# Kernel tuning notes

Measured on AMD Instinct MI355X. Metric: run time of the kernel, lower is better.

The kernel has to match this reference:

```python
import jax, jax.numpy as jnp
import numpy as np

B, S, D, H, N = 8, 1024, 1024, 16, 16  # batch, seq, hidden, heads, num_ns_tokens
HD = D // H


def setup_inputs() -> dict:
    key = jax.random.key(0)
    ks = jax.random.split(key, 8)
    s = 0.02
    return {
        "x": jax.random.normal(ks[0], (B, S, D), jnp.float32),
        "Wq_shared": jax.random.normal(ks[1], (D, D), jnp.float32) * s,
        "Wk_shared": jax.random.normal(ks[2], (D, D), jnp.float32) * s,
        "Wv_shared": jax.random.normal(ks[3], (D, D), jnp.float32) * s,
        "Wq_ded": jax.random.normal(ks[4], (N, D, D), jnp.float32) * s,
        "Wk_ded": jax.random.normal(ks[5], (N, D, D), jnp.float32) * s,
        "Wv_ded": jax.random.normal(ks[6], (N, D, D), jnp.float32) * s,
        "Wo": jax.random.normal(ks[7], (D, D), jnp.float32) * s,
    }


def reference(x, Wq_shared, Wk_shared, Wv_shared, Wq_ded, Wk_ded, Wv_ded, Wo):
    b, s, d = x.shape
    n = Wq_ded.shape[0]

    def proj(Ws, Wd):
        shared = x @ Ws                                   # [b,s,d]
        ded = jnp.einsum('bnd,ndo->bno', x[:, :n], Wd)    # first n tokens use dedicated weights
        return jnp.concatenate([ded, shared[:, n:]], axis=1)

    q = proj(Wq_shared, Wq_ded).reshape(b, s, H, HD)
    k = proj(Wk_shared, Wk_ded).reshape(b, s, H, HD)
    v = proj(Wv_shared, Wv_ded).reshape(b, s, H, HD)

    scores = jnp.einsum('bqhd,bkhd->bhqk', q, k) / jnp.sqrt(jnp.float32(HD))
    causal = jnp.tril(jnp.ones((s, s), dtype=bool))
    scores = jnp.where(causal, scores, jnp.float32(-1e9))
    attn = jax.nn.softmax(scores, axis=-1)
    out = jnp.einsum('bhqk,bkhd->bqhd', attn, v).reshape(b, s, d)
    output = out @ Wo
    return (output, k, v)
```

## Files before the change

kernel.cpp:

```cpp
#include <hip/hip_runtime.h>
#include <cstdint>


typedef unsigned short u16;
typedef __attribute__((ext_vector_type(8)))  __bf16 bf16x8;
typedef __attribute__((ext_vector_type(8)))  u16    u16x8;
typedef __attribute__((ext_vector_type(4)))  float  f32x4;

#define BSD   (8u * 1024u * 1024u)
#define QSCALE 0.18033688011112042f

__device__ __forceinline__ u16 f2bf(float f) {
    unsigned u = __builtin_bit_cast(unsigned, f);
    u += 0x7fffu + ((u >> 16) & 1u);
    return (u16)(u >> 16);
}

__device__ __forceinline__ unsigned pack_bf2(float p0, float p1) {
    return __builtin_amdgcn_perm(__builtin_bit_cast(unsigned, p1),
                                 __builtin_bit_cast(unsigned, p0), 0x07060302u);
}

__device__ __forceinline__ void gl_lds16(const void* g, void* l) {
    __builtin_amdgcn_global_load_lds(
        (const __attribute__((address_space(1))) unsigned*)g,
        (__attribute__((address_space(3))) unsigned*)l, 16, 0, 0);
}

__global__ __launch_bounds__(256) void cvt_fused(
        const float* __restrict__ Wq, const float* __restrict__ Wk,
        const float* __restrict__ Wv, const float* __restrict__ Wo,
        u16* __restrict__ WTcat, u16* __restrict__ WoT,
        const float4* __restrict__ x, u16* __restrict__ xb) {
    __shared__ float t[32][33];
    int z = blockIdx.z;
    if (z < 4) {
        const float* src = (z == 0) ? Wq : (z == 1) ? Wk : (z == 2) ? Wv : Wo;
        u16* dst = (z < 3) ? (WTcat + (size_t)z * 1024 * 1024) : WoT;
        int k0 = blockIdx.x * 32, n0 = blockIdx.y * 32;
        int xx = threadIdx.x & 31, yy = threadIdx.x >> 5;
#pragma unroll
        for (int i = 0; i < 4; ++i)
            t[yy + 8 * i][xx] = src[(size_t)(k0 + yy + 8 * i) * 1024 + n0 + xx];
        __syncthreads();
#pragma unroll
        for (int i = 0; i < 4; ++i)
            dst[(size_t)(n0 + yy + 8 * i) * 1024 + k0 + xx] = f2bf(t[xx][yy + 8 * i]);
    } else {
        int lb = (z - 4) * 1024 + blockIdx.y * 32 + blockIdx.x;
        int i = lb * 256 + threadIdx.x;
        float4 v = x[i];
        ushort4 o;
        o.x = f2bf(v.x); o.y = f2bf(v.y); o.z = f2bf(v.z); o.w = f2bf(v.w);
        ((ushort4*)xb)[i] = o;
    }
}

template <int MODE>
__global__ __launch_bounds__(256) void gemm128(
        const u16* __restrict__ A, const u16* __restrict__ Bt,
        float* __restrict__ fout, u16* __restrict__ q_attn,
        u16* __restrict__ k_attn) {
    const int K = 1024;
    __shared__ u16 As[128 * 64];
    __shared__ u16 Bs[128 * 64];
    int tid = threadIdx.x;
    int wave = tid >> 6, lane = tid & 63;
    int m0 = blockIdx.y * 128, n0 = blockIdx.x * 128;
    int wm = wave & 1, wn = wave >> 1;
    int lr = lane & 15, kg = lane >> 4;

    f32x4 acc[4][4] = {};

    for (int k0 = 0; k0 < K; k0 += 64) {
        __syncthreads();
#pragma unroll
        for (int j = 0; j < 4; ++j) {
            int ci = j * 256 + tid;
            int row = ci >> 3, cg = (ci & 7) ^ (row & 7);
            gl_lds16(A  + (size_t)(m0 + row) * K + k0 + cg * 8, As + ci * 8);
            gl_lds16(Bt + (size_t)(n0 + row) * K + k0 + cg * 8, Bs + ci * 8);
        }
        __syncthreads();
#pragma unroll
        for (int ks = 0; ks < 2; ++ks) {
            bf16x8 af[4], bf[4];
#pragma unroll
            for (int i = 0; i < 4; ++i) {
                int row = wm * 64 + i * 16 + lr;
                af[i] = __builtin_bit_cast(bf16x8,
                    *(const u16x8*)&As[row * 64 + (((ks * 4 + kg) ^ (row & 7)) * 8)]);
            }
#pragma unroll
            for (int j = 0; j < 4; ++j) {
                int row = wn * 64 + j * 16 + lr;
                bf[j] = __builtin_bit_cast(bf16x8,
                    *(const u16x8*)&Bs[row * 64 + (((ks * 4 + kg) ^ (row & 7)) * 8)]);
            }
#pragma unroll
            for (int i = 0; i < 4; ++i)
#pragma unroll
                for (int j = 0; j < 4; ++j)
                    acc[i][j] = __builtin_amdgcn_mfma_f32_16x16x32_bf16(
                        af[i], bf[j], acc[i][j], 0, 0, 0);
        }
    }

    if (MODE == 1) {
#pragma unroll
        for (int i = 0; i < 4; ++i) {
            int mbase = m0 + wm * 64 + i * 16 + kg * 4;
#pragma unroll
            for (int j = 0; j < 4; ++j) {
                int col = n0 + wn * 64 + j * 16 + lr;
#pragma unroll
                for (int r = 0; r < 4; ++r)
                    fout[(size_t)(mbase + r) * 1024 + col] = acc[i][j][r];
            }
        }
    } else {
        int matId = n0 >> 10;
        int ncol0 = (n0 & 1023) + wn * 64;
#pragma unroll
        for (int i = 0; i < 4; ++i) {
            int mbase = m0 + wm * 64 + i * 16 + kg * 4;
#pragma unroll
            for (int j = 0; j < 4; ++j) {
                int col = ncol0 + j * 16 + lr;
#pragma unroll
                for (int r = 0; r < 4; ++r) {
                    int mm = mbase + r;
                    float v = acc[i][j][r];
                    size_t idx = (size_t)mm * 1024 + col;
                    if (matId == 0) {
                        q_attn[idx] = f2bf(v * QSCALE);
                    } else if (matId == 1) {
                        fout[(size_t)BSD + idx] = v;
                        k_attn[idx] = f2bf(v);
                    } else {
                        fout[(size_t)2 * BSD + idx] = v;
                    }
                }
            }
        }
    }
}

__global__ __launch_bounds__(256) void ded_partial(
        const float* __restrict__ x, const float* __restrict__ Wq,
        const float* __restrict__ Wk, const float* __restrict__ Wv,
        float* __restrict__ part) {
    int dc = blockIdx.x, n = blockIdx.y, mat = blockIdx.z;
    const float* W = ((mat == 0) ? Wq : (mat == 1) ? Wk : Wv) +
                     (size_t)n * 1024 * 1024;
    __shared__ float xs[8 * 128];
    int t = threadIdx.x;
    for (int i = t; i < 1024; i += 256) {
        int b = i >> 7, d = i & 127;
        xs[i] = x[((size_t)b * 1024 + n) * 1024 + dc * 128 + d];
    }
    __syncthreads();
    int o0 = t * 4;
    float4 acc[8];
#pragma unroll
    for (int b = 0; b < 8; ++b) acc[b] = make_float4(0.f, 0.f, 0.f, 0.f);
    for (int d = 0; d < 128; d += 4) {
        float4 w0 = *(const float4*)&W[(size_t)(dc * 128 + d + 0) * 1024 + o0];
        float4 w1 = *(const float4*)&W[(size_t)(dc * 128 + d + 1) * 1024 + o0];
        float4 w2 = *(const float4*)&W[(size_t)(dc * 128 + d + 2) * 1024 + o0];
        float4 w3 = *(const float4*)&W[(size_t)(dc * 128 + d + 3) * 1024 + o0];
#pragma unroll
        for (int b = 0; b < 8; ++b) {
            float x0 = xs[b * 128 + d], x1 = xs[b * 128 + d + 1];
            float x2 = xs[b * 128 + d + 2], x3 = xs[b * 128 + d + 3];
            acc[b].x += x0 * w0.x + x1 * w1.x + x2 * w2.x + x3 * w3.x;
            acc[b].y += x0 * w0.y + x1 * w1.y + x2 * w2.y + x3 * w3.y;
            acc[b].z += x0 * w0.z + x1 * w1.z + x2 * w2.z + x3 * w3.z;
            acc[b].w += x0 * w0.w + x1 * w1.w + x2 * w2.w + x3 * w3.w;
        }
    }
#pragma unroll
    for (int b = 0; b < 8; ++b)
        *(float4*)&part[(size_t)(((mat * 8 + dc) * 8 + b) * 16 + n) * 1024 + o0] = acc[b];
}

__global__ __launch_bounds__(256) void fix_vt(
        const float* __restrict__ part, float* __restrict__ d_out,
        u16* __restrict__ q_attn, u16* __restrict__ k_attn,
        const float* __restrict__ vf, u16* __restrict__ vT) {
    __shared__ float t[64][65];
    int bid = blockIdx.x;
    int tid = threadIdx.x;

    if (bid < 384) {
        int mat = bid >> 7, b = (bid >> 4) & 7, n = bid & 15;
        int o0 = tid * 4;
        float v[4] = {0.f, 0.f, 0.f, 0.f};
        for (int dc = 0; dc < 8; ++dc) {
            float4 p = *(const float4*)&part[(size_t)(((mat * 8 + dc) * 8 + b) * 16 + n) * 1024 + o0];
            v[0] += p.x; v[1] += p.y; v[2] += p.z; v[3] += p.w;
        }
#pragma unroll
        for (int j = 0; j < 4; ++j) {
            int col = o0 + j;
            size_t idx = ((size_t)b * 1024 + n) * 1024 + col;
            if (mat == 0) {
                q_attn[idx] = f2bf(v[j] * QSCALE);
            } else if (mat == 1) {
                d_out[(size_t)BSD + idx] = v[j];
                k_attn[idx] = f2bf(v[j]);
            } else {
                d_out[(size_t)2 * BSD + idx] = v[j];
                int h = col >> 6, hd = col & 63;
                vT[((size_t)((b * 16 + h) * 64 + hd)) * 1024 + n] = f2bf(v[j]);
            }
        }
        return;
    }

    int id = bid - 384;
    int st = id & 15, h = (id >> 4) & 15, b = id >> 8;
    int cg = tid & 15, sl = tid >> 4;
#pragma unroll
    for (int p = 0; p < 4; ++p) {
        int s = p * 16 + sl;
        float4 v = *(const float4*)&vf[
            ((size_t)(b * 1024 + st * 64 + s)) * 1024 + h * 64 + cg * 4];
        t[cg * 4 + 0][s] = v.x;
        t[cg * 4 + 1][s] = v.y;
        t[cg * 4 + 2][s] = v.z;
        t[cg * 4 + 3][s] = v.w;
    }
    __syncthreads();
    int hd = tid >> 2, sc = (tid & 3) * 16;
    if (st == 0 && sc == 0) return;
    u16* dst = vT + ((size_t)((b * 16 + h) * 64 + hd)) * 1024 + st * 64 + sc;
#pragma unroll
    for (int c = 0; c < 4; ++c) {
        ushort4 o;
        o.x = f2bf(t[hd][sc + c * 4 + 0]);
        o.y = f2bf(t[hd][sc + c * 4 + 1]);
        o.z = f2bf(t[hd][sc + c * 4 + 2]);
        o.w = f2bf(t[hd][sc + c * 4 + 3]);
        *(ushort4*)(dst + c * 4) = o;
    }
}

__global__ __launch_bounds__(256) void attn(
        const u16* __restrict__ q_attn, const u16* __restrict__ k_attn,
        const u16* __restrict__ vT, u16* __restrict__ O) {
    int qt = 7 - blockIdx.x;
    int h = blockIdx.y, b = blockIdx.z;
    const u16* Qg = q_attn + ((size_t)(b * 1024) + qt * 128) * 1024 + h * 64;
    const u16* Kg = k_attn + ((size_t)(b * 1024)) * 1024 + h * 64;
    const u16* Vg = vT + (size_t)((b * 16 + h) * 64) * 1024;

    __shared__ u16 Qs[128 * 64];
    __shared__ u16 Ks[64 * 64];
    __shared__ u16 Vs[64 * 64];
    __shared__ u16 Ps[128 * 64];
    __shared__ float red[4 * 32];

    int tid = threadIdx.x, wave = tid >> 6, lane = tid & 63;
    int lr = lane & 15, kg = lane >> 4;

#pragma unroll
    for (int j = 0; j < 4; ++j) {
        int ci = j * 256 + tid;
        int row = ci >> 3, cg = (ci & 7) ^ (row & 7);
        gl_lds16(Qg + (size_t)row * 1024 + cg * 8, Qs + ci * 8);
    }

    float l_acc[2] = {0.f, 0.f};
    f32x4 oacc[2][4] = {};

    int nkt = 2 * qt + 2;
    for (int kt = 0; kt < nkt; ++kt) {
        __syncthreads();
#pragma unroll
        for (int j = 0; j < 2; ++j) {
            int ci = j * 256 + tid;
            int row = ci >> 3, cg = (ci & 7) ^ (row & 7);
            gl_lds16(Kg + (size_t)(kt * 64 + row) * 1024 + cg * 8, Ks + ci * 8);
            gl_lds16(Vg + (size_t)row * 1024 + kt * 64 + cg * 8, Vs + ci * 8);
        }
        __syncthreads();

        bool wactive = (qt * 128 + wave * 32 + 31) >= kt * 64;
        if (wactive) {
            f32x4 sacc[4][2] = {};
#pragma unroll
            for (int ks = 0; ks < 2; ++ks) {
                bf16x8 af[4], bq[2];
#pragma unroll
                for (int mi = 0; mi < 4; ++mi) {
                    int row = mi * 16 + lr;
                    af[mi] = __builtin_bit_cast(bf16x8,
                        *(const u16x8*)&Ks[row * 64 + (((ks * 4 + kg) ^ (row & 7)) * 8)]);
                }
#pragma unroll
                for (int nj = 0; nj < 2; ++nj) {
                    int qr = wave * 32 + nj * 16 + lr;
                    bq[nj] = __builtin_bit_cast(bf16x8,
                        *(const u16x8*)&Qs[qr * 64 + (((ks * 4 + kg) ^ (qr & 7)) * 8)]);
                }
#pragma unroll
                for (int mi = 0; mi < 4; ++mi)
#pragma unroll
                    for (int nj = 0; nj < 2; ++nj)
                        sacc[mi][nj] = __builtin_amdgcn_mfma_f32_16x16x32_bf16(
                            af[mi], bq[nj], sacc[mi][nj], 0, 0, 0);
            }

            if (kt >= 2 * qt) {
#pragma unroll
                for (int mi = 0; mi < 4; ++mi)
#pragma unroll
                    for (int nj = 0; nj < 2; ++nj)
#pragma unroll
                        for (int r = 0; r < 4; ++r) {
                            int kk_g = kt * 64 + mi * 16 + kg * 4 + r;
                            int q_g  = qt * 128 + wave * 32 + nj * 16 + lr;
                            if (kk_g > q_g) sacc[mi][nj][r] = -1e30f;
                        }
            }

#pragma unroll
            for (int nj = 0; nj < 2; ++nj) {
                int q = wave * 32 + nj * 16 + lr;
                float lsum = 0.f;
#pragma unroll
                for (int mi = 0; mi < 4; ++mi) {
                    float p0 = __builtin_amdgcn_exp2f(sacc[mi][nj][0]);
                    float p1 = __builtin_amdgcn_exp2f(sacc[mi][nj][1]);
                    float p2 = __builtin_amdgcn_exp2f(sacc[mi][nj][2]);
                    float p3 = __builtin_amdgcn_exp2f(sacc[mi][nj][3]);
                    lsum += (p0 + p1) + (p2 + p3);
                    int kkc = mi * 2 + (kg >> 1);
                    int off = q * 64 + ((kkc ^ (q & 7)) * 8) + (kg & 1) * 4;
                    uint2 w2;
                    w2.x = pack_bf2(p0, p1);
                    w2.y = pack_bf2(p2, p3);
                    *(uint2*)&Ps[off] = w2;
                }
                l_acc[nj] += lsum;
            }

#pragma unroll
            for (int ks = 0; ks < 2; ++ks) {
                bf16x8 ap[2], bv[4];
#pragma unroll
                for (int mi = 0; mi < 2; ++mi) {
                    int q = wave * 32 + mi * 16 + lr;
                    ap[mi] = __builtin_bit_cast(bf16x8,
                        *(const u16x8*)&Ps[q * 64 + (((ks * 4 + kg) ^ (q & 7)) * 8)]);
                }
#pragma unroll
                for (int nj = 0; nj < 4; ++nj) {
                    int hd = nj * 16 + lr;
                    bv[nj] = __builtin_bit_cast(bf16x8,
                        *(const u16x8*)&Vs[hd * 64 + (((ks * 4 + kg) ^ (hd & 7)) * 8)]);
                }
#pragma unroll
                for (int mi = 0; mi < 2; ++mi)
#pragma unroll
                    for (int nj = 0; nj < 4; ++nj)
                        oacc[mi][nj] = __builtin_amdgcn_mfma_f32_16x16x32_bf16(
                            ap[mi], bv[nj], oacc[mi][nj], 0, 0, 0);
            }
        }
    }

#pragma unroll
    for (int nj = 0; nj < 2; ++nj) {
        float l = l_acc[nj];
        l += __shfl_xor(l, 16);
        l += __shfl_xor(l, 32);
        if (kg == 0) red[wave * 32 + nj * 16 + lr] = l;
    }
#pragma unroll
    for (int mi = 0; mi < 2; ++mi) {
        f32x4 lv = *(f32x4*)&red[wave * 32 + mi * 16 + kg * 4];
        f32x4 rv;
#pragma unroll
        for (int r = 0; r < 4; ++r) rv[r] = __builtin_amdgcn_rcpf(lv[r]);
#pragma unroll
        for (int nj = 0; nj < 4; ++nj)
#pragma unroll
            for (int r = 0; r < 4; ++r) {
                int q_local = wave * 32 + mi * 16 + kg * 4 + r;
                size_t row = (size_t)b * 1024 + qt * 128 + q_local;
                O[row * 1024 + h * 64 + nj * 16 + lr] =
                    f2bf(oacc[mi][nj][r] * rv[r]);
            }
    }
}

extern "C" void kernel_launch(void* const* d_in, const int* in_sizes, int n_in,
                              void* d_out, int out_size, void* d_ws, size_t ws_size,
                              hipStream_t stream) {
    const float* x   = (const float*)d_in[0];
    const float* Wq  = (const float*)d_in[1];
    const float* Wk  = (const float*)d_in[2];
    const float* Wv  = (const float*)d_in[3];
    const float* Wqd = (const float*)d_in[4];
    const float* Wkd = (const float*)d_in[5];
    const float* Wvd = (const float*)d_in[6];
    const float* Wo  = (const float*)d_in[7];
    float* out = (float*)d_out;

    char* ws = (char*)d_ws;
    u16*   WTcat  = (u16*)(ws);
    u16*   WoT    = (u16*)(ws + 6291456);
    u16*   xb     = (u16*)(ws + 8388608);
    u16*   q_attn = (u16*)(ws + 25165824);
    u16*   k_attn = (u16*)(ws + 41943040);
    u16*   vT     = (u16*)(ws + 58720256);
    u16*   Ow     = (u16*)(ws + 75497472);
    float* part   = (float*)(ws + 92274688);

    cvt_fused<<<dim3(32, 32, 12), 256, 0, stream>>>(
        Wq, Wk, Wv, Wo, WTcat, WoT, (const float4*)x, xb);
    gemm128<0><<<dim3(24, 64), 256, 0, stream>>>(xb, WTcat, out, q_attn, k_attn);
    ded_partial<<<dim3(8, 16, 3), 256, 0, stream>>>(x, Wqd, Wkd, Wvd, part);
    fix_vt<<<dim3(2432), 256, 0, stream>>>(
        part, out, q_attn, k_attn, out + (size_t)2 * BSD, vT);
    attn<<<dim3(8, 16, 8), 256, 0, stream>>>(q_attn, k_attn, vT, Ow);
    gemm128<1><<<dim3(8, 64), 256, 0, stream>>>(Ow, WoT, out, nullptr, nullptr);
}
```

Before: 462.7 us.

## Replace GEMM with 8-wave double-buffered 128x256 tile ping-pong pipeline

Replaces the 4-wave 128x128 single-buffered GEMM with an 8-wave 128x256 tile kernel that double-buffers LDS. Global-to-LDS loads for the next K-step are split into four phases and interleaved with MFMA quarters, gated by explicit vmcnt waits, barriers and setprio. The aim is to hide global load latency behind compute and raise reuse per tile. In exchange it uses more LDS (96KB per block, which limits occupancy) and more barriers per K-step, and the hand-tuned waitcnt schedule is fragile.

Measured after the change: 474.3 us. 2.5% more time.

```diff
diff --git a/kernel.cpp b/kernel.cpp
--- a/kernel.cpp
+++ b/kernel.cpp
@@ -26,6 +26,9 @@
         (const __attribute__((address_space(1))) unsigned*)g,
         (__attribute__((address_space(3))) unsigned*)l, 16, 0, 0);
 }
+
+#define FENCE asm volatile("" ::: "memory")
+#define WAITV(n) asm volatile("s_waitcnt vmcnt(" #n ")" ::: "memory")
 
 __global__ __launch_bounds__(256) void cvt_fused(
         const float* __restrict__ Wq, const float* __restrict__ Wk,
@@ -56,81 +59,113 @@
     }
 }
 
+#define LDfrag(BUF, bufi, row, ks)                                            \
+    __builtin_bit_cast(bf16x8, *(const u16x8*)&BUF[bufi]                      \
+        [(row) * 64 + ((((ks) * 4 + kg) ^ ((row) & 7)) * 8)])
+
+#define PH(bufi, mh, nh, STAGE_STMT, GATE_STMT) do {                          \
+    bf16x8 af_[2][2], bq_[2][2];                                              \
+    _Pragma("unroll") for (int mi = 0; mi < 2; ++mi) {                        \
+        int arow = wm * 64 + (mh) * 32 + mi * 16 + lr;                        \
+        _Pragma("unroll") for (int ks = 0; ks < 2; ++ks)                      \
+            af_[mi][ks] = LDfrag(As, bufi, arow, ks);                         \
+    }                                                                         \
+    _Pragma("unroll") for (int ni = 0; ni < 2; ++ni) {                        \
+        int brow = wn * 64 + (nh) * 32 + ni * 16 + lr;                        \
+        _Pragma("unroll") for (int ks = 0; ks < 2; ++ks)                      \
+            bq_[ni][ks] = LDfrag(Bs, bufi, brow, ks);                         \
+    }                                                                         \
+    STAGE_STMT;                                                               \
+    GATE_STMT;                                                                \
+    FENCE; __builtin_amdgcn_s_barrier(); FENCE;                               \
+    asm volatile("s_waitcnt lgkmcnt(0)" ::: "memory");                        \
+    __builtin_amdgcn_s_setprio(1);                                            \
+    _Pragma("unroll") for (int ks = 0; ks < 2; ++ks)                          \
+    _Pragma("unroll") for (int mi = 0; mi < 2; ++mi)                          \
+    _Pragma("unroll") for (int ni = 0; ni < 2; ++ni)                          \
+        acc[(mh) * 2 + mi][(nh) * 2 + ni] =                                   \
+            __builtin_amdgcn_mfma_f32_16x16x32_bf16(                          \
+                af_[mi][ks], bq_[ni][ks],                                     \
+                acc[(mh) * 2 + mi][(nh) * 2 + ni], 0, 0, 0);                  \
+    __builtin_amdgcn_s_setprio(0);                                            \
+    FENCE; __builtin_amdgcn_s_barrier(); FENCE;                               \
+} while (0)
+
 template <int MODE>
-__global__ __launch_bounds__(256) void gemm128(
+__global__ __launch_bounds__(512, 2) void gemm8p(
         const u16* __restrict__ A, const u16* __restrict__ Bt,
         float* __restrict__ fout, u16* __restrict__ q_attn,
         u16* __restrict__ k_attn) {
-    const int K = 1024;
-    __shared__ u16 As[128 * 64];
-    __shared__ u16 Bs[128 * 64];
+    const int K = 1024, nt = 16;
+    __shared__ u16 As[2][128 * 64];
+    __shared__ u16 Bs[2][256 * 64];
     int tid = threadIdx.x;
-    int wave = tid >> 6, lane = tid & 63;
-    int m0 = blockIdx.y * 128, n0 = blockIdx.x * 128;
-    int wm = wave & 1, wn = wave >> 1;
+    int w = tid >> 6, lane = tid & 63;
+    int m0 = blockIdx.y * 128, n0 = blockIdx.x * 256;
+    int wm = w & 1, wn = w >> 1;
     int lr = lane & 15, kg = lane >> 4;
 
     f32x4 acc[4][4] = {};
 
-    for (int k0 = 0; k0 < K; k0 += 64) {
-        __syncthreads();
-#pragma unroll
-        for (int j = 0; j < 4; ++j) {
-            int ci = j * 256 + tid;
+    auto stageA = [&](int buf, int half, int t) {
+        int ci = ((w & 3) << 6) + lane + ((w >> 2) << 9) + (half << 8);
+        int row = ci >> 3, cg = (ci & 7) ^ (row & 7);
+        gl_lds16(A + (size_t)(m0 + row) * K + t * 64 + cg * 8, &As[buf][ci * 8]);
+    };
+    auto stageB = [&](int buf, int half, int t) {
+#pragma unroll
+        for (int j = 0; j < 2; ++j) {
+            int u = w + 8 * j;
+            int ci = ((u >> 2) << 9) + ((u & 3) << 6) + lane + (half << 8);
             int row = ci >> 3, cg = (ci & 7) ^ (row & 7);
-            gl_lds16(A  + (size_t)(m0 + row) * K + k0 + cg * 8, As + ci * 8);
-            gl_lds16(Bt + (size_t)(n0 + row) * K + k0 + cg * 8, Bs + ci * 8);
-        }
-        __syncthreads();
-#pragma unroll
-        for (int ks = 0; ks < 2; ++ks) {
-            bf16x8 af[4], bf[4];
-#pragma unroll
-            for (int i = 0; i < 4; ++i) {
-                int row = wm * 64 + i * 16 + lr;
-                af[i] = __builtin_bit_cast(bf16x8,
-                    *(const u16x8*)&As[row * 64 + (((ks * 4 + kg) ^ (row & 7)) * 8)]);
-            }
-#pragma unroll
-            for (int j = 0; j < 4; ++j) {
-                int row = wn * 64 + j * 16 + lr;
-                bf[j] = __builtin_bit_cast(bf16x8,
-                    *(const u16x8*)&Bs[row * 64 + (((ks * 4 + kg) ^ (row & 7)) * 8)]);
-            }
-#pragma unroll
-            for (int i = 0; i < 4; ++i)
-#pragma unroll
-                for (int j = 0; j < 4; ++j)
-                    acc[i][j] = __builtin_amdgcn_mfma_f32_16x16x32_bf16(
-                        af[i], bf[j], acc[i][j], 0, 0, 0);
-        }
-    }
+            gl_lds16(Bt + (size_t)(n0 + row) * K + t * 64 + cg * 8, &Bs[buf][ci * 8]);
+        }
+    };
+
+    stageA(0, 0, 0);
+    stageB(0, 0, 0);
+    stageA(0, 1, 0);
+    stageB(0, 1, 0);
+    WAITV(3);
+    FENCE; __builtin_amdgcn_s_barrier(); FENCE;
+
+    for (int t = 0; t < nt - 1; ++t) {
+        int cur = t & 1, nxt = cur ^ 1;
+        PH(cur, 0, 0, stageA(nxt, 0, t + 1), WAITV(3));
+        PH(cur, 1, 0, stageB(nxt, 0, t + 1), WAITV(3));
+        PH(cur, 1, 1, stageA(nxt, 1, t + 1), ((void)0));
+        PH(cur, 0, 1, stageB(nxt, 1, t + 1), WAITV(3));
+    }
+    PH(1, 0, 0, ((void)0), WAITV(2));
+    PH(1, 1, 0, ((void)0), WAITV(0));
+    PH(1, 1, 1, ((void)0), ((void)0));
+    PH(1, 0, 1, ((void)0), ((void)0));
 
     if (MODE == 1) {
 #pragma unroll
-        for (int i = 0; i < 4; ++i) {
-            int mbase = m0 + wm * 64 + i * 16 + kg * 4;
-#pragma unroll
-            for (int j = 0; j < 4; ++j) {
-                int col = n0 + wn * 64 + j * 16 + lr;
+        for (int am = 0; am < 4; ++am) {
+            int mbase = m0 + wm * 64 + am * 16 + kg * 4;
+#pragma unroll
+            for (int bn = 0; bn < 4; ++bn) {
+                int col = n0 + wn * 64 + bn * 16 + lr;
 #pragma unroll
                 for (int r = 0; r < 4; ++r)
-                    fout[(size_t)(mbase + r) * 1024 + col] = acc[i][j][r];
+                    fout[(size_t)(mbase + r) * 1024 + col] = acc[am][bn][r];
             }
         }
     } else {
         int matId = n0 >> 10;
         int ncol0 = (n0 & 1023) + wn * 64;
 #pragma unroll
-        for (int i = 0; i < 4; ++i) {
-            int mbase = m0 + wm * 64 + i * 16 + kg * 4;
-#pragma unroll
-            for (int j = 0; j < 4; ++j) {
-                int col = ncol0 + j * 16 + lr;
+        for (int am = 0; am < 4; ++am) {
+            int mbase = m0 + wm * 64 + am * 16 + kg * 4;
+#pragma unroll
+            for (int bn = 0; bn < 4; ++bn) {
+                int col = ncol0 + bn * 16 + lr;
 #pragma unroll
                 for (int r = 0; r < 4; ++r) {
                     int mm = mbase + r;
-                    float v = acc[i][j][r];
+                    float v = acc[am][bn][r];
                     size_t idx = (size_t)mm * 1024 + col;
                     if (matId == 0) {
                         q_attn[idx] = f2bf(v * QSCALE);
@@ -421,10 +456,10 @@
 
     cvt_fused<<<dim3(32, 32, 12), 256, 0, stream>>>(
         Wq, Wk, Wv, Wo, WTcat, WoT, (const float4*)x, xb);
-    gemm128<0><<<dim3(24, 64), 256, 0, stream>>>(xb, WTcat, out, q_attn, k_attn);
+    gemm8p<0><<<dim3(12, 64), 512, 0, stream>>>(xb, WTcat, out, q_attn, k_attn);
     ded_partial<<<dim3(8, 16, 3), 256, 0, stream>>>(x, Wqd, Wkd, Wvd, part);
     fix_vt<<<dim3(2432), 256, 0, stream>>>(
         part, out, q_attn, k_attn, out + (size_t)2 * BSD, vT);
     attn<<<dim3(8, 16, 8), 256, 0, stream>>>(q_attn, k_attn, vT, Ow);
-    gemm128<1><<<dim3(8, 64), 256, 0, stream>>>(Ow, WoT, out, nullptr, nullptr);
-}
+    gemm8p<1><<<dim3(4, 64), 512, 0, stream>>>(Ow, WoT, out, nullptr, nullptr);
+}
```
